# Optimization experiments

Measured on AMD Instinct MI355X. Metric: run time of the kernel, lower is better.

Reference implementation:

```python
import jax, jax.numpy as jnp
import numpy as np

H = 1024      # hidden_size
V = 50257     # output_size (vocab)


def setup_inputs() -> dict:
    key = jax.random.key(0)
    ks = jax.random.split(key, 9)
    s = 1.0 / np.sqrt(H)
    return {
        "input_ids": jax.random.randint(ks[0], (1,), 0, V, dtype=jnp.int64)
        if jax.config.jax_enable_x64 else jax.random.randint(ks[0], (1,), 0, V, dtype=jnp.int32),
        "hidden": jax.random.normal(ks[1], (1, 1, H), dtype=jnp.float32),
        "emb": jax.random.normal(ks[2], (V, H), dtype=jnp.float32),
        "W_ih": jax.random.uniform(ks[3], (3 * H, H), jnp.float32, -s, s),
        "W_hh": jax.random.uniform(ks[4], (3 * H, H), jnp.float32, -s, s),
        "b_ih": jax.random.uniform(ks[5], (3 * H,), jnp.float32, -s, s),
        "b_hh": jax.random.uniform(ks[6], (3 * H,), jnp.float32, -s, s),
        "W_out": jax.random.uniform(ks[7], (V, H), jnp.float32, -s, s),
        "b_out": jax.random.uniform(ks[8], (V,), jnp.float32, -s, s),
    }


def gru_cell(x, h, W_ih, W_hh, b_ih, b_hh):
    # x, h: [B, H]; PyTorch GRU gate ordering: r, z, n
    gi = x @ W_ih.T + b_ih           # [B, 3H]
    gh = h @ W_hh.T + b_hh           # [B, 3H]
    i_r, i_z, i_n = jnp.split(gi, 3, axis=-1)
    h_r, h_z, h_n = jnp.split(gh, 3, axis=-1)
    r = jax.nn.sigmoid(i_r + h_r)
    z = jax.nn.sigmoid(i_z + h_z)
    n = jnp.tanh(i_n + r * h_n)
    return (1.0 - z) * n + z * h


def reference(input_ids, hidden, emb, W_ih, W_hh, b_ih, b_hh, W_out, b_out):
    # embedding lookup -> [1, 1, H] (seq=1, batch=1)
    x = emb[input_ids].reshape(1, 1, H)
    x = jax.nn.relu(x)
    # single-step, single-layer GRU (n_layers = 1 in the original intent)
    h_new = gru_cell(x[0], hidden[0], W_ih, W_hh, b_ih, b_hh)   # [1, H]
    hidden_out = h_new[None]                                    # [1, 1, H]
    logits = h_new @ W_out.T + b_out                            # [1, V]
    logp = jax.nn.log_softmax(logits, axis=-1)
    return logp, hidden_out
```

## Files before the change

### kernel.cpp

```cpp
#include <hip/hip_runtime.h>
#include <math.h>

#define H 1024
#define V 50257
#define NB_TILES 3142
#define NB_FINAL 64

__device__ __forceinline__ float wave_reduce_sum(float v) {
#pragma unroll
    for (int off = 32; off >= 1; off >>= 1)
        v += __shfl_xor(v, off, 64);
    return v;
}

__device__ __forceinline__ void sm_merge(float& m, float& s, float mi, float si) {
    if (mi > m) {
        s = s * expf(m - mi) + si;
        m = mi;
    } else if (si > 0.f) {
        s += si * expf(mi - m);
    }
}

__global__ __launch_bounds__(256) void gru_fused_kernel(
    const int* __restrict__ ids, const float* __restrict__ emb,
    const float* __restrict__ hidden,
    const float* __restrict__ W_ih, const float* __restrict__ W_hh,
    const float* __restrict__ b_ih, const float* __restrict__ b_hh,
    float* __restrict__ hnew, float* __restrict__ out_hidden)
{
    const int j = blockIdx.x;
    const int t = threadIdx.x;
    const int wave = t >> 6;
    const int lane = t & 63;

    const int id = ids[0];

    float4 x4 = ((const float4*)(emb + (size_t)id * H))[t];
    const float4 h4 = ((const float4*)hidden)[t];
    float4 wi[3], wh[3];
#pragma unroll
    for (int g = 0; g < 3; ++g) {
        wi[g] = ((const float4*)(W_ih + ((size_t)g * H + j) * H))[t];
        wh[g] = ((const float4*)(W_hh + ((size_t)g * H + j) * H))[t];
    }

    x4.x = fmaxf(x4.x, 0.f); x4.y = fmaxf(x4.y, 0.f);
    x4.z = fmaxf(x4.z, 0.f); x4.w = fmaxf(x4.w, 0.f);

    float acc[6];
#pragma unroll
    for (int g = 0; g < 3; ++g) {
        acc[2*g]   = wi[g].x * x4.x + wi[g].y * x4.y + wi[g].z * x4.z + wi[g].w * x4.w;
        acc[2*g+1] = wh[g].x * h4.x + wh[g].y * h4.y + wh[g].z * h4.z + wh[g].w * h4.w;
    }
#pragma unroll
    for (int g = 0; g < 6; ++g) acc[g] = wave_reduce_sum(acc[g]);

    __shared__ float red[4][6];
    if (lane == 0) {
#pragma unroll
        for (int g = 0; g < 6; ++g) red[wave][g] = acc[g];
    }
    __syncthreads();
    if (t == 0) {
        float tt[6];
#pragma unroll
        for (int g = 0; g < 6; ++g)
            tt[g] = red[0][g] + red[1][g] + red[2][g] + red[3][g];
        const float ir  = tt[0] + b_ih[j],        hr_ = tt[1] + b_hh[j];
        const float iz  = tt[2] + b_ih[H + j],    hz  = tt[3] + b_hh[H + j];
        const float in_ = tt[4] + b_ih[2*H + j],  hn  = tt[5] + b_hh[2*H + j];
        const float r = 1.f / (1.f + expf(-(ir + hr_)));
        const float z = 1.f / (1.f + expf(-(iz + hz)));
        const float n = tanhf(in_ + r * hn);
        const float h = hidden[j];
        const float o = (1.f - z) * n + z * h;
        hnew[j] = o;
        out_hidden[j] = o;
    }
}

__global__ __launch_bounds__(256) void logits_kernel(
    const float* __restrict__ hnew, const float* __restrict__ W_out,
    const float* __restrict__ b_out, float* __restrict__ logits,
    float* __restrict__ pmax, float* __restrict__ psum)
{
    __shared__ float wm[4], wsv[4];
    const int wave = threadIdx.x >> 6;
    const int lane = threadIdx.x & 63;
    const int base = blockIdx.x * 16 + wave * 4;

    float4 hreg[4];
#pragma unroll
    for (int it = 0; it < 4; ++it)
        hreg[it] = ((const float4*)hnew)[it * 64 + lane];

    float m = -INFINITY, s = 0.f;

    if (base + 3 < V) {
        float4 wreg[4][4];
#pragma unroll
        for (int r = 0; r < 4; ++r) {
            const float4* w = (const float4*)(W_out + (size_t)(base + r) * H);
#pragma unroll
            for (int it = 0; it < 4; ++it)
                wreg[r][it] = w[it * 64 + lane];
        }
        float acc[4];
#pragma unroll
        for (int r = 0; r < 4; ++r) {
            acc[r] = 0.f;
#pragma unroll
            for (int it = 0; it < 4; ++it)
                acc[r] += wreg[r][it].x * hreg[it].x + wreg[r][it].y * hreg[it].y
                        + wreg[r][it].z * hreg[it].z + wreg[r][it].w * hreg[it].w;
        }
#pragma unroll
        for (int r = 0; r < 4; ++r) acc[r] = wave_reduce_sum(acc[r]);
        if (lane == 0) {
#pragma unroll
            for (int r = 0; r < 4; ++r) {
                const float logit = acc[r] + b_out[base + r];
                logits[base + r] = logit;
                sm_merge(m, s, logit, 1.f);
            }
        }
    } else {
        for (int r = 0; r < 4; ++r) {
            const int row = base + r;
            if (row >= V) break;
            const float4* w = (const float4*)(W_out + (size_t)row * H);
            float acc = 0.f;
#pragma unroll
            for (int it = 0; it < 4; ++it) {
                const float4 w4 = w[it * 64 + lane];
                acc += w4.x * hreg[it].x + w4.y * hreg[it].y
                     + w4.z * hreg[it].z + w4.w * hreg[it].w;
            }
            acc = wave_reduce_sum(acc);
            if (lane == 0) {
                const float logit = acc + b_out[row];
                logits[row] = logit;
                sm_merge(m, s, logit, 1.f);
            }
        }
    }

    if (lane == 0) { wm[wave] = m; wsv[wave] = s; }
    __syncthreads();
    if (threadIdx.x == 0) {
        float M = wm[0], S = wsv[0];
#pragma unroll
        for (int w2 = 1; w2 < 4; ++w2) sm_merge(M, S, wm[w2], wsv[w2]);
        pmax[blockIdx.x] = M;
        psum[blockIdx.x] = S;
    }
}

__global__ __launch_bounds__(256) void finalize_kernel(
    const float* __restrict__ pmax, const float* __restrict__ psum,
    float* __restrict__ out)
{
    __shared__ float wm[4], wsv[4];
    __shared__ float total_s;
    const int tid = threadIdx.x;

    float m = -INFINITY, s = 0.f;
    for (int i = tid; i < NB_TILES; i += 256)
        sm_merge(m, s, pmax[i], psum[i]);
#pragma unroll
    for (int off = 32; off >= 1; off >>= 1) {
        const float mo = __shfl_xor(m, off, 64);
        const float so = __shfl_xor(s, off, 64);
        sm_merge(m, s, mo, so);
    }
    if ((tid & 63) == 0) { wm[tid >> 6] = m; wsv[tid >> 6] = s; }
    __syncthreads();
    if (tid == 0) {
        float M = wm[0], S = wsv[0];
#pragma unroll
        for (int w2 = 1; w2 < 4; ++w2) sm_merge(M, S, wm[w2], wsv[w2]);
        total_s = M + logf(S);
    }
    __syncthreads();
    const float t = total_s;
    for (int v = blockIdx.x * 256 + tid; v < V; v += NB_FINAL * 256)
        out[v] -= t;
}

extern "C" void kernel_launch(void* const* d_in, const int* in_sizes, int n_in,
                              void* d_out, int out_size, void* d_ws, size_t ws_size,
                              hipStream_t stream) {
    const int*   ids    = (const int*)  d_in[0];
    const float* hidden = (const float*)d_in[1];
    const float* emb    = (const float*)d_in[2];
    const float* W_ih   = (const float*)d_in[3];
    const float* W_hh   = (const float*)d_in[4];
    const float* b_ih   = (const float*)d_in[5];
    const float* b_hh   = (const float*)d_in[6];
    const float* W_out  = (const float*)d_in[7];
    const float* b_out  = (const float*)d_in[8];

    float* out = (float*)d_out;

    float* ws   = (float*)d_ws;
    float* hnew = ws;
    float* pmax = ws + H;
    float* psum = pmax + NB_TILES;

    gru_fused_kernel<<<H, 256, 0, stream>>>(ids, emb, hidden, W_ih, W_hh,
                                            b_ih, b_hh, hnew, out + V);
    logits_kernel<<<NB_TILES, 256, 0, stream>>>(hnew, W_out, b_out, out,
                                                pmax, psum);
    finalize_kernel<<<NB_FINAL, 256, 0, stream>>>(pmax, psum, out);
}
```

Baseline: 51.42 us.

## Make logits kernel persistent with double-buffered register prefetch of W_out tiles

Replaces the one-tile-per-block logits kernel with 512 persistent blocks that loop over tiles, prefetching the next tile's W_out rows into a second register buffer while computing the current one. This also shrinks the partial max/sum arrays the finalize kernel must merge. The finalize subtraction is vectorized to float4 with a scalar tail. The risk is that fewer resident waves and higher register use reduce memory-level parallelism for the bandwidth-bound W_out stream.

```diff
diff --git a/kernel.cpp b/kernel.cpp
--- a/kernel.cpp
+++ b/kernel.cpp
@@ -3,7 +3,8 @@
 
 #define H 1024
 #define V 50257
-#define NB_TILES 3142
+#define NTILES 3142
+#define NBLK 512
 #define NB_FINAL 64
 
 __device__ __forceinline__ float wave_reduce_sum(float v) {
@@ -81,7 +82,48 @@
     }
 }
 
-__global__ __launch_bounds__(256) void logits_kernel(
+
+#define LOADT(W, tile) do {                                                   \
+    const int _b = (tile) * 16 + wave * 4;                                    \
+    _Pragma("unroll")                                                         \
+    for (int _r = 0; _r < 4; ++_r) {                                          \
+        const int _row = (_b + _r < V) ? (_b + _r) : (V - 1);                 \
+        const float4* _w = (const float4*)(W_out + (size_t)_row * H);         \
+        _Pragma("unroll")                                                     \
+        for (int _it = 0; _it < 4; ++_it) W[_r][_it] = _w[_it * 64 + lane];   \
+    }                                                                         \
+} while (0)
+
+#define COMPUTET(W, tile) do {                                                \
+    const int _b = (tile) * 16 + wave * 4;                                    \
+    float _acc[4];                                                            \
+    _Pragma("unroll")                                                         \
+    for (int _r = 0; _r < 4; ++_r) {                                          \
+        _acc[_r] = W[_r][0].x * hreg[0].x + W[_r][0].y * hreg[0].y            \
+                 + W[_r][0].z * hreg[0].z + W[_r][0].w * hreg[0].w            \
+                 + W[_r][1].x * hreg[1].x + W[_r][1].y * hreg[1].y            \
+                 + W[_r][1].z * hreg[1].z + W[_r][1].w * hreg[1].w            \
+                 + W[_r][2].x * hreg[2].x + W[_r][2].y * hreg[2].y            \
+                 + W[_r][2].z * hreg[2].z + W[_r][2].w * hreg[2].w            \
+                 + W[_r][3].x * hreg[3].x + W[_r][3].y * hreg[3].y            \
+                 + W[_r][3].z * hreg[3].z + W[_r][3].w * hreg[3].w;           \
+    }                                                                         \
+    _Pragma("unroll")                                                         \
+    for (int _r = 0; _r < 4; ++_r) _acc[_r] = wave_reduce_sum(_acc[_r]);      \
+    if (lane == 0) {                                                          \
+        _Pragma("unroll")                                                     \
+        for (int _r = 0; _r < 4; ++_r) {                                      \
+            const int _row = _b + _r;                                         \
+            if (_row < V) {                                                   \
+                const float _lg = _acc[_r] + b_out[_row];                     \
+                logits[_row] = _lg;                                           \
+                sm_merge(m, s, _lg, 1.f);                                     \
+            }                                                                 \
+        }                                                                     \
+    }                                                                         \
+} while (0)
+
+__global__ __launch_bounds__(256) void logits_persistent_kernel(
     const float* __restrict__ hnew, const float* __restrict__ W_out,
     const float* __restrict__ b_out, float* __restrict__ logits,
     float* __restrict__ pmax, float* __restrict__ psum)
@@ -89,7 +131,7 @@
     __shared__ float wm[4], wsv[4];
     const int wave = threadIdx.x >> 6;
     const int lane = threadIdx.x & 63;
-    const int base = blockIdx.x * 16 + wave * 4;
+    const int bid  = blockIdx.x;
 
     float4 hreg[4];
 #pragma unroll
@@ -98,53 +140,21 @@
 
     float m = -INFINITY, s = 0.f;
 
-    if (base + 3 < V) {
-        float4 wreg[4][4];
-#pragma unroll
-        for (int r = 0; r < 4; ++r) {
-            const float4* w = (const float4*)(W_out + (size_t)(base + r) * H);
-#pragma unroll
-            for (int it = 0; it < 4; ++it)
-                wreg[r][it] = w[it * 64 + lane];
-        }
-        float acc[4];
-#pragma unroll
-        for (int r = 0; r < 4; ++r) {
-            acc[r] = 0.f;
-#pragma unroll
-            for (int it = 0; it < 4; ++it)
-                acc[r] += wreg[r][it].x * hreg[it].x + wreg[r][it].y * hreg[it].y
-                        + wreg[r][it].z * hreg[it].z + wreg[r][it].w * hreg[it].w;
-        }
-#pragma unroll
-        for (int r = 0; r < 4; ++r) acc[r] = wave_reduce_sum(acc[r]);
-        if (lane == 0) {
-#pragma unroll
-            for (int r = 0; r < 4; ++r) {
-                const float logit = acc[r] + b_out[base + r];
-                logits[base + r] = logit;
-                sm_merge(m, s, logit, 1.f);
-            }
-        }
-    } else {
-        for (int r = 0; r < 4; ++r) {
-            const int row = base + r;
-            if (row >= V) break;
-            const float4* w = (const float4*)(W_out + (size_t)row * H);
-            float acc = 0.f;
-#pragma unroll
-            for (int it = 0; it < 4; ++it) {
-                const float4 w4 = w[it * 64 + lane];
-                acc += w4.x * hreg[it].x + w4.y * hreg[it].y
-                     + w4.z * hreg[it].z + w4.w * hreg[it].w;
-            }
-            acc = wave_reduce_sum(acc);
-            if (lane == 0) {
-                const float logit = acc + b_out[row];
-                logits[row] = logit;
-                sm_merge(m, s, logit, 1.f);
-            }
-        }
+    float4 wA[4][4], wB[4][4];
+    int t = bid;
+    LOADT(wA, t);
+    for (;;) {
+        const int tn = t + NBLK;
+        const bool vn = tn < NTILES;
+        if (vn) LOADT(wB, tn);
+        COMPUTET(wA, t);
+        if (!vn) break;
+        const int tn2 = tn + NBLK;
+        const bool vn2 = tn2 < NTILES;
+        if (vn2) LOADT(wA, tn2);
+        COMPUTET(wB, tn);
+        if (!vn2) break;
+        t = tn2;
     }
 
     if (lane == 0) { wm[wave] = m; wsv[wave] = s; }
@@ -153,8 +163,8 @@
         float M = wm[0], S = wsv[0];
 #pragma unroll
         for (int w2 = 1; w2 < 4; ++w2) sm_merge(M, S, wm[w2], wsv[w2]);
-        pmax[blockIdx.x] = M;
-        psum[blockIdx.x] = S;
+        pmax[bid] = M;
+        psum[bid] = S;
     }
 }
 
@@ -167,7 +177,7 @@
     const int tid = threadIdx.x;
 
     float m = -INFINITY, s = 0.f;
-    for (int i = tid; i < NB_TILES; i += 256)
+    for (int i = tid; i < NBLK; i += 256)
         sm_merge(m, s, pmax[i], psum[i]);
 #pragma unroll
     for (int off = 32; off >= 1; off >>= 1) {
@@ -185,8 +195,15 @@
     }
     __syncthreads();
     const float t = total_s;
-    for (int v = blockIdx.x * 256 + tid; v < V; v += NB_FINAL * 256)
-        out[v] -= t;
+
+    float4* out4 = (float4*)out;
+    const int n4 = V / 4;
+    for (int i = blockIdx.x * 256 + tid; i < n4; i += NB_FINAL * 256) {
+        float4 v = out4[i];
+        v.x -= t; v.y -= t; v.z -= t; v.w -= t;
+        out4[i] = v;
+    }
+    if (blockIdx.x == 0 && tid == 0) out[V - 1] -= t;
 }
 
 extern "C" void kernel_launch(void* const* d_in, const int* in_sizes, int n_in,
@@ -207,11 +224,11 @@
     float* ws   = (float*)d_ws;
     float* hnew = ws;
     float* pmax = ws + H;
-    float* psum = pmax + NB_TILES;
+    float* psum = pmax + NBLK;
 
     gru_fused_kernel<<<H, 256, 0, stream>>>(ids, emb, hidden, W_ih, W_hh,
                                             b_ih, b_hh, hnew, out + V);
-    logits_kernel<<<NB_TILES, 256, 0, stream>>>(hnew, W_out, b_out, out,
-                                                pmax, psum);
+    logits_persistent_kernel<<<NBLK, 256, 0, stream>>>(hnew, W_out, b_out, out,
+                                                       pmax, psum);
     finalize_kernel<<<NB_FINAL, 256, 0, stream>>>(pmax, psum, out);
 }
```

Measured after the change: 48.24 us. 1.07x faster.
